# Performance work log

Measured on AMD Instinct MI355X. Metric: run time of the kernel, lower is better.

The kernel has to match this reference:

```python
import jax, jax.numpy as jnp
import numpy as np

N_NODES = 100000
N_EDGES = 3200000
HID = 128
NUM_ATTR = 10000
K = 3
EPS = 1e-5


def setup_inputs() -> dict:
    key = jax.random.key(0)
    ks = jax.random.split(key, 8)
    x_idx = jax.random.randint(ks[0], (N_NODES,), 0, NUM_ATTR)
    edge_index = jax.random.randint(ks[1], (2, N_EDGES), 0, N_NODES)
    edge_weight = jax.random.uniform(ks[2], (N_EDGES,), dtype=jnp.float32)
    emb = jax.random.normal(ks[3], (NUM_ATTR, HID), dtype=jnp.float32) * 0.1
    Wt = jax.random.normal(ks[4], (K, HID, HID), dtype=jnp.float32) * (1.0 / np.sqrt(HID))
    bt = jnp.zeros((K, HID), jnp.float32)
    Wc = jax.random.normal(ks[5], (K, 2 * HID, HID), dtype=jnp.float32) * (1.0 / np.sqrt(2 * HID))
    bc = jnp.zeros((K, HID), jnp.float32)
    cg_gamma = jnp.ones((K, HID), jnp.float32)
    cg_beta = jnp.zeros((K, HID), jnp.float32)
    cg_alpha = jnp.ones((K, HID), jnp.float32)
    gn_gamma = jnp.ones((K - 1, HID), jnp.float32)
    gn_beta = jnp.zeros((K - 1, HID), jnp.float32)
    gn_alpha = jnp.ones((K - 1, HID), jnp.float32)
    return dict(x_idx=x_idx, edge_index=edge_index, edge_weight=edge_weight, emb=emb,
                Wt=Wt, bt=bt, Wc=Wc, bc=bc, cg_gamma=cg_gamma, cg_beta=cg_beta,
                cg_alpha=cg_alpha, gn_gamma=gn_gamma, gn_beta=gn_beta, gn_alpha=gn_alpha)


def graph_norm(x, gamma, beta, alpha):
    # GraphNorm over node dim: out = gamma*(x - alpha*mean)/sqrt(var+eps) + beta
    mean = jnp.mean(x, axis=0, keepdims=True)
    sub = x - alpha * mean
    var = jnp.mean(sub * sub, axis=0, keepdims=True)
    return gamma * sub * jax.lax.rsqrt(var + EPS) + beta


def build_mean_adj_weights(edge_index, edge_weight, n_nodes):
    # aggr='mean': w_e = edge_weight_e / deg[row_e], deg from row sums (deg<0.5 -> +1)
    row = edge_index[0]
    deg = jax.ops.segment_sum(edge_weight, row, num_segments=n_nodes)
    deg = jnp.where(deg < 0.5, deg + 1.0, deg)
    inv_deg = 1.0 / deg
    return edge_weight * inv_deg[row]


def conv_layer(x_, row, col, w, Wt, bt, Wc, bc, g, b, a):
    h = jax.nn.relu(x_ @ Wt + bt)                                   # [N, HID]
    m = jax.ops.segment_sum(w[:, None] * h[col], row, num_segments=x_.shape[0])  # adj @ h
    m = graph_norm(m, g, b, a)
    return jnp.concatenate([m, x_], axis=-1) @ Wc + bc


def reference(x_idx, edge_index, edge_weight, emb, Wt, bt, Wc, bc,
              cg_gamma, cg_beta, cg_alpha, gn_gamma, gn_beta, gn_alpha):
    row, col = edge_index[0], edge_index[1]
    w = build_mean_adj_weights(edge_index, edge_weight, x_idx.shape[0])
    x = emb[x_idx]  # embedding lookup; dropout p=0 -> identity
    for i in range(K - 1):
        x = conv_layer(x, row, col, w, Wt[i], bt[i], Wc[i], bc[i],
                       cg_gamma[i], cg_beta[i], cg_alpha[i])
        x = graph_norm(x, gn_gamma[i], gn_beta[i], gn_alpha[i])
        x = jax.nn.relu(x)
    x = conv_layer(x, row, col, w, Wt[K - 1], bt[K - 1], Wc[K - 1], bc[K - 1],
                   cg_gamma[K - 1], cg_beta[K - 1], cg_alpha[K - 1])
    return x
```

## Files before the change

### kernel.cpp

```cpp
#include <hip/hip_runtime.h>
#include <cstdio>


#define HID 128

typedef __attribute__((ext_vector_type(8))) short short8;
typedef __attribute__((ext_vector_type(4))) float floatx4;
typedef __attribute__((ext_vector_type(8))) _Float16 half8;
typedef __attribute__((ext_vector_type(2))) _Float16 half2v;

__device__ __forceinline__ unsigned short f2bf(float f) {
    unsigned u = __float_as_uint(f);
    unsigned r = (u + 0x7FFFu + ((u >> 16) & 1u)) >> 16;
    return (unsigned short)r;
}
__device__ __forceinline__ float bflo(unsigned u) { return __uint_as_float(u << 16); }
__device__ __forceinline__ float bfhi(unsigned u) { return __uint_as_float(u & 0xFFFF0000u); }

#define NB 512
#define RPB 196
#define CAPB 8192
#define TILE_A 2048

__global__ __launch_bounds__(256) void k_binA(
    const int* __restrict__ row, const int* __restrict__ col,
    const float* __restrict__ ew, int2* __restrict__ binned,
    unsigned* __restrict__ cursor, int E) {
    __shared__ int2 stag[TILE_A];
    __shared__ unsigned short bof[TILE_A];
    __shared__ unsigned hist[NB], scanned[NB], bump[NB];
    __shared__ int delta[NB];
    __shared__ unsigned scanw[256];
    int t = threadIdx.x;
    int tileBase = blockIdx.x * TILE_A;
    int tcnt = min(TILE_A, E - tileBase);

    hist[t] = 0; hist[t + 256] = 0;
    __syncthreads();

    int myb[8]; int2 myv[8];
#pragma unroll
    for (int i = 0; i < 8; ++i) {
        int idx = t + i * 256;
        if (idx < tcnt) {
            int e = tileBase + idx;
            int r = row[e];
            int c = col[e];
            float w = ew[e];
            int b = r / RPB;
            int rl = r - b * RPB;
            myb[i] = b;
            myv[i] = make_int2((rl << 17) | c, __float_as_int(w));
            atomicAdd(&hist[b], 1u);
        } else {
            myb[i] = -1;
            myv[i] = make_int2(0, 0);
        }
    }
    __syncthreads();

    unsigned h0 = hist[2 * t], h1 = hist[2 * t + 1];
    unsigned p = h0 + h1;
    scanw[t] = p;
    __syncthreads();
    for (int o = 1; o < 256; o <<= 1) {
        unsigned x = (t >= o) ? scanw[t - o] : 0u;
        __syncthreads();
        scanw[t] += x;
        __syncthreads();
    }
    unsigned excl = scanw[t] - p;
    scanned[2 * t] = excl;          bump[2 * t] = excl;
    scanned[2 * t + 1] = excl + h0; bump[2 * t + 1] = excl + h0;
    __syncthreads();

#pragma unroll
    for (int j = 0; j < 2; ++j) {
        int b = t + j * 256;
        unsigned c = hist[b];
        if (c) {
            unsigned old = atomicAdd(&cursor[b], c);
            delta[b] = (int)((unsigned)b * CAPB + old) - (int)scanned[b];
        }
    }
    __syncthreads();

#pragma unroll
    for (int i = 0; i < 8; ++i) {
        if (myb[i] >= 0) {
            unsigned s = atomicAdd(&bump[myb[i]], 1u);
            stag[s] = myv[i];
            bof[s] = (unsigned short)myb[i];
        }
    }
    __syncthreads();

    for (int i = t; i < tcnt; i += 256) {
        int b = bof[i];
        int dst = delta[b] + i;
        if (dst < (b + 1) * CAPB) binned[dst] = stag[i];
    }
}

__global__ void k_bscan(const unsigned* __restrict__ cursor, unsigned* __restrict__ outbase) {
    __shared__ unsigned scanw[256];
    int t = threadIdx.x;
    unsigned h0 = min(cursor[2 * t], (unsigned)CAPB);
    unsigned h1 = min(cursor[2 * t + 1], (unsigned)CAPB);
    unsigned p = h0 + h1;
    scanw[t] = p;
    __syncthreads();
    for (int o = 1; o < 256; o <<= 1) {
        unsigned x = (t >= o) ? scanw[t - o] : 0u;
        __syncthreads();
        scanw[t] += x;
        __syncthreads();
    }
    unsigned excl = scanw[t] - p;
    outbase[2 * t] = excl;
    outbase[2 * t + 1] = excl + h0;
}

__global__ __launch_bounds__(256) void k_binB(
    const int2* __restrict__ binned, const unsigned* __restrict__ cursor,
    const unsigned* __restrict__ outbase, int2* __restrict__ edge_s,
    unsigned* __restrict__ endp, unsigned* __restrict__ cntg, int N) {
    __shared__ unsigned hist[256], bump[256], scanw[256];
    __shared__ float wsum[256], inv[256];
    int b = blockIdx.x, t = threadIdx.x;
    size_t base_in = (size_t)b * CAPB;
    unsigned cntb = min(cursor[b], (unsigned)CAPB);
    unsigned outb = outbase[b];

    hist[t] = 0;
    wsum[t] = 0.f;
    __syncthreads();
    for (unsigned i = t; i < cntb; i += 256) {
        int2 v = binned[base_in + i];
        unsigned rl = ((unsigned)v.x) >> 17;
        atomicAdd(&hist[rl], 1u);
        atomicAdd(&wsum[rl], __int_as_float(v.y));
    }
    __syncthreads();

    unsigned h = hist[t];
    scanw[t] = h;
    __syncthreads();
    for (int o = 1; o < 256; o <<= 1) {
        unsigned x = (t >= o) ? scanw[t - o] : 0u;
        __syncthreads();
        scanw[t] += x;
        __syncthreads();
    }
    unsigned excl = scanw[t] - h;
    bump[t] = excl;
    float d = wsum[t];
    d = (d < 0.5f) ? d + 1.0f : d;
    inv[t] = 1.0f / d;
    int grow = b * RPB + t;
    if (t < RPB && grow < N) {
        endp[grow] = outb + excl + h;
        cntg[grow] = h;
    }
    __syncthreads();

    for (unsigned i = t; i < cntb; i += 256) {
        int2 v = binned[base_in + i];
        unsigned rl = ((unsigned)v.x) >> 17;
        unsigned pos = outb + atomicAdd(&bump[rl], 1u);
        float w = __int_as_float(v.y) * inv[rl];
        edge_s[pos] = make_int2(v.x & 0x1FFFF, __float_as_int(w));
    }
}

__global__ void k_prepw(const float* __restrict__ Wt, const float* __restrict__ Wc,
                        unsigned short* __restrict__ WtT, unsigned short* __restrict__ WcT) {
    int tid = blockIdx.x * blockDim.x + threadIdx.x;
    const int T1 = 3 * 128 * 128;
    const int T2 = 3 * 256 * 128;
    if (tid < T1) {
        int l = tid >> 14, rem = tid & 16383;
        int n = rem >> 7, k = rem & 127;
        WtT[tid] = f2bf(Wt[l * 16384 + k * 128 + n]);
    } else if (tid < T1 + T2) {
        int t2 = tid - T1;
        int l = t2 >> 15, rem = t2 & 32767;
        int n = rem >> 8, k = rem & 255;
        WcT[t2] = f2bf(Wc[l * 32768 + k * 128 + n]);
    }
}

#define GM_ROWS 128
#define LDSP 136

__global__ __launch_bounds__(256) void k_gemm(
    const float* __restrict__ X1, const int* __restrict__ G1,
    const float* __restrict__ AB1, int relu1, int x1_f16,
    const float* __restrict__ X2, const int* __restrict__ G2,
    const float* __restrict__ AB2, int relu2,
    const unsigned short* __restrict__ Wn, int Kpitch, int nstage,
    const float* __restrict__ bias, void* __restrict__ Y, int relu_out, int out_bf16,
    float* __restrict__ Sout, int N) {
    __shared__ unsigned short Ws[128 * LDSP];
    __shared__ unsigned short Xs[128 * LDSP];
    __shared__ float sred[4][256];
    int t = threadIdx.x;
    int rowBase = blockIdx.x * GM_ROWS;
    int lane = t & 63, wave = t >> 6;
    int quad = lane >> 4, l16 = lane & 15;

    floatx4 acc[2][8];
#pragma unroll
    for (int i = 0; i < 2; ++i)
#pragma unroll
        for (int j = 0; j < 8; ++j) acc[i][j] = (floatx4){0.f, 0.f, 0.f, 0.f};

    int kg = (t & 15) * 8;
    int r0 = t >> 4;

    for (int s = 0; s < nstage; ++s) {
        const float* Xp = s ? X2 : X1;
        const int* Gp = s ? G2 : G1;
        const float* ABp = s ? AB2 : AB1;
        int rl = s ? relu2 : relu1;
        int koff = s * 128;

#pragma unroll
        for (int j = 0; j < 8; ++j) {
            int n = r0 + 16 * j;
            *(short8*)&Ws[n * LDSP + kg] =
                *(const short8*)&Wn[(size_t)n * Kpitch + koff + kg];
        }
        floatx4 Av0 = {1.f, 1.f, 1.f, 1.f}, Av1 = Av0;
        floatx4 Bv0 = {0.f, 0.f, 0.f, 0.f}, Bv1 = Bv0;
        if (ABp) {
            Av0 = *(const floatx4*)&ABp[kg];
            Av1 = *(const floatx4*)&ABp[kg + 4];
            Bv0 = *(const floatx4*)&ABp[HID + kg];
            Bv1 = *(const floatx4*)&ABp[HID + kg + 4];
        }
#pragma unroll
        for (int j = 0; j < 8; ++j) {
            int r = r0 + 16 * j;
            int grow = rowBase + r;
            floatx4 x0 = {0.f, 0.f, 0.f, 0.f}, x1 = x0;
            if (grow < N) {
                size_t srow = Gp ? (size_t)Gp[grow] : (size_t)grow;
                if (x1_f16 && s == 0) {
                    half8 mv = *(const half8*)&((const _Float16*)X1)[srow * HID + kg];
#pragma unroll
                    for (int c = 0; c < 4; ++c) {
                        x0[c] = (float)mv[c];
                        x1[c] = (float)mv[c + 4];
                    }
                } else {
                    x0 = *(const floatx4*)&Xp[srow * HID + kg];
                    x1 = *(const floatx4*)&Xp[srow * HID + kg + 4];
                }
            }
            if (ABp) {
#pragma unroll
                for (int c = 0; c < 4; ++c) {
                    x0[c] = fmaf(x0[c], Av0[c], Bv0[c]);
                    x1[c] = fmaf(x1[c], Av1[c], Bv1[c]);
                }
                if (rl) {
#pragma unroll
                    for (int c = 0; c < 4; ++c) {
                        x0[c] = fmaxf(x0[c], 0.f);
                        x1[c] = fmaxf(x1[c], 0.f);
                    }
                }
            }
            short8 st;
            st[0] = (short)f2bf(x0[0]); st[1] = (short)f2bf(x0[1]);
            st[2] = (short)f2bf(x0[2]); st[3] = (short)f2bf(x0[3]);
            st[4] = (short)f2bf(x1[0]); st[5] = (short)f2bf(x1[1]);
            st[6] = (short)f2bf(x1[2]); st[7] = (short)f2bf(x1[3]);
            *(short8*)&Xs[r * LDSP + kg] = st;
        }
        __syncthreads();

#pragma unroll
        for (int ks = 0; ks < 4; ++ks) {
            int kb = ks * 32 + quad * 8;
            short8 a0 = *(const short8*)&Xs[(wave * 32 + l16) * LDSP + kb];
            short8 a1 = *(const short8*)&Xs[(wave * 32 + 16 + l16) * LDSP + kb];
#pragma unroll
            for (int ni = 0; ni < 8; ++ni) {
                short8 b = *(const short8*)&Ws[(ni * 16 + l16) * LDSP + kb];
                acc[0][ni] = __builtin_amdgcn_mfma_f32_16x16x32_bf16(a0, b, acc[0][ni], 0, 0, 0);
                acc[1][ni] = __builtin_amdgcn_mfma_f32_16x16x32_bf16(a1, b, acc[1][ni], 0, 0, 0);
            }
        }
        __syncthreads();
    }

    float s1[8], s2[8];
#pragma unroll
    for (int ni = 0; ni < 8; ++ni) { s1[ni] = 0.f; s2[ni] = 0.f; }

#pragma unroll
    for (int mi = 0; mi < 2; ++mi) {
#pragma unroll
        for (int ni = 0; ni < 8; ++ni) {
            int gcol = ni * 16 + l16;
            float bv = bias[gcol];
#pragma unroll
            for (int reg = 0; reg < 4; ++reg) {
                int grow = rowBase + wave * 32 + mi * 16 + quad * 4 + reg;
                if (grow < N) {
                    float v = acc[mi][ni][reg] + bv;
                    if (relu_out) v = fmaxf(v, 0.f);
                    s1[ni] += v;
                    s2[ni] += v * v;
                    if (out_bf16)
                        ((unsigned short*)Y)[(size_t)grow * HID + gcol] = f2bf(v);
                    else
                        ((float*)Y)[(size_t)grow * HID + gcol] = v;
                }
            }
        }
    }

    if (Sout) {
#pragma unroll
        for (int ni = 0; ni < 8; ++ni) {
            s1[ni] += __shfl_xor(s1[ni], 16);
            s1[ni] += __shfl_xor(s1[ni], 32);
            s2[ni] += __shfl_xor(s2[ni], 16);
            s2[ni] += __shfl_xor(s2[ni], 32);
        }
        if (lane < 16) {
#pragma unroll
            for (int ni = 0; ni < 8; ++ni) {
                sred[wave][ni * 16 + l16] = s1[ni];
                sred[wave][128 + ni * 16 + l16] = s2[ni];
            }
        }
        __syncthreads();
        float v = sred[0][t & 255];
        if (t < 256) {
            v = sred[0][t] + sred[1][t] + sred[2][t] + sred[3][t];
            atomicAdd(&Sout[(blockIdx.x & 15) * 256 + t], v);
        }
    }
}

#define AGG_R 4

__global__ __launch_bounds__(256) void k_agg(
    const unsigned short* __restrict__ H, const int2* __restrict__ es,
    const unsigned* __restrict__ endp, const unsigned* __restrict__ cnt,
    _Float16* __restrict__ Mh, float* __restrict__ Spart, int N) {
    __shared__ float sb[4][256];
    int t = threadIdx.x;
    int wv = t >> 6, lane = t & 63;
    int grp = lane >> 4;
    int l16 = lane & 15;
    const uint4* __restrict__ H4 = (const uint4*)H;
    int rowBase = blockIdx.x * (4 * AGG_R) + wv * AGG_R;
    int fo = l16 * 8 + grp * 2;
    float s1a = 0.f, s1b = 0.f, s2a = 0.f, s2b = 0.f;

    for (int j = 0; j < AGG_R; ++j) {
        int rowi = rowBase + j;
        if (rowi >= N) break;
        unsigned e = endp[rowi];
        unsigned p = e - cnt[rowi];

        float acc[8];
#pragma unroll
        for (int i = 0; i < 8; ++i) acc[i] = 0.f;

        for (; p + 15 < e; p += 16) {
            int2 ee[4];
#pragma unroll
            for (int q = 0; q < 4; ++q) ee[q] = es[p + 4 * q + grp];
            uint4 hh[4];
#pragma unroll
            for (int q = 0; q < 4; ++q)
                hh[q] = H4[(size_t)ee[q].x * 16 + l16];
            __builtin_amdgcn_sched_barrier(0);
#pragma unroll
            for (int q = 0; q < 4; ++q) {
                float w = __int_as_float(ee[q].y);
                acc[0] = fmaf(w, bflo(hh[q].x), acc[0]);
                acc[1] = fmaf(w, bfhi(hh[q].x), acc[1]);
                acc[2] = fmaf(w, bflo(hh[q].y), acc[2]);
                acc[3] = fmaf(w, bfhi(hh[q].y), acc[3]);
                acc[4] = fmaf(w, bflo(hh[q].z), acc[4]);
                acc[5] = fmaf(w, bfhi(hh[q].z), acc[5]);
                acc[6] = fmaf(w, bflo(hh[q].w), acc[6]);
                acc[7] = fmaf(w, bfhi(hh[q].w), acc[7]);
            }
        }
        for (; p < e; p += 4) {
            unsigned idx = p + grp;
            int2 e0 = make_int2(0, 0);
            if (idx < e) e0 = es[idx];
            uint4 h = H4[(size_t)e0.x * 16 + l16];
            float w = __int_as_float(e0.y);
            acc[0] = fmaf(w, bflo(h.x), acc[0]);
            acc[1] = fmaf(w, bfhi(h.x), acc[1]);
            acc[2] = fmaf(w, bflo(h.y), acc[2]);
            acc[3] = fmaf(w, bfhi(h.y), acc[3]);
            acc[4] = fmaf(w, bflo(h.z), acc[4]);
            acc[5] = fmaf(w, bfhi(h.z), acc[5]);
            acc[6] = fmaf(w, bflo(h.w), acc[6]);
            acc[7] = fmaf(w, bfhi(h.w), acc[7]);
        }

#pragma unroll
        for (int i = 0; i < 8; ++i) {
            acc[i] += __shfl_xor(acc[i], 16);
            acc[i] += __shfl_xor(acc[i], 32);
        }
        float va = (grp & 2) ? ((grp & 1) ? acc[6] : acc[4])
                             : ((grp & 1) ? acc[2] : acc[0]);
        float vb = (grp & 2) ? ((grp & 1) ? acc[7] : acc[5])
                             : ((grp & 1) ? acc[3] : acc[1]);
        half2v st;
        st[0] = (_Float16)va;
        st[1] = (_Float16)vb;
        *(half2v*)&Mh[(size_t)rowi * HID + fo] = st;
        s1a += va; s1b += vb;
        s2a += va * va; s2b += vb * vb;
    }

    sb[wv][fo] = s1a;
    sb[wv][fo + 1] = s1b;
    sb[wv][128 + fo] = s2a;
    sb[wv][128 + fo + 1] = s2b;
    __syncthreads();
    {
        float v = sb[0][t] + sb[1][t] + sb[2][t] + sb[3][t];
        atomicAdd(&Spart[(blockIdx.x & 15) * 256 + t], v);
    }
}

__global__ void k_finalize(const float* __restrict__ S, const float* __restrict__ gamma,
                           const float* __restrict__ beta, const float* __restrict__ alpha,
                           float* __restrict__ AB, float invN) {
    int f = threadIdx.x;
    float sum = 0.f, sq = 0.f;
#pragma unroll
    for (int c = 0; c < 16; ++c) {
        sum += S[c * 256 + f];
        sq += S[c * 256 + 128 + f];
    }
    float mu = sum * invN;
    float ex2 = sq * invN;
    float a = alpha[f];
    float var = ex2 - 2.f * a * mu * mu + a * a * mu * mu;
    float rs = rsqrtf(var + 1e-5f);
    float A = gamma[f] * rs;
    float B = beta[f] - A * a * mu;
    AB[f] = A;
    AB[HID + f] = B;
}

extern "C" void kernel_launch(void* const* d_in, const int* in_sizes, int n_in,
                              void* d_out, int out_size, void* d_ws, size_t ws_size,
                              hipStream_t stream) {
    const int*   x_idx = (const int*)d_in[0];
    const int*   ei    = (const int*)d_in[1];
    const float* ew    = (const float*)d_in[2];
    const float* emb   = (const float*)d_in[3];
    const float* Wt    = (const float*)d_in[4];
    const float* bt    = (const float*)d_in[5];
    const float* Wc    = (const float*)d_in[6];
    const float* bc    = (const float*)d_in[7];
    const float* cg_g  = (const float*)d_in[8];
    const float* cg_b  = (const float*)d_in[9];
    const float* cg_a  = (const float*)d_in[10];
    const float* gn_g  = (const float*)d_in[11];
    const float* gn_b  = (const float*)d_in[12];
    const float* gn_a  = (const float*)d_in[13];
    const int N = in_sizes[0];
    const int E = in_sizes[2];
    const int* row = ei;
    const int* col = ei + E;

    char* ws = (char*)d_ws;
    size_t off = 0;
    auto alloc = [&](size_t bytes) -> void* {
        size_t o = (off + 511) & ~(size_t)511;
        off = o + bytes;
        return (void*)(ws + o);
    };
    const int SSTRIDE = 16 * 256;
    unsigned* cursor = (unsigned*)alloc(NB * 4);
    float*    Spart  = (float*)alloc(5 * SSTRIDE * 4);
    size_t zero_end = off;
    unsigned* outbase = (unsigned*)alloc(NB * 4);
    unsigned* endp    = (unsigned*)alloc((size_t)N * 4);
    unsigned* cnt     = (unsigned*)alloc((size_t)N * 4);
    float*    AB      = (float*)alloc(5 * 256 * 4);
    unsigned short* WtT = (unsigned short*)alloc((size_t)3 * 128 * 128 * 2);
    unsigned short* WcT = (unsigned short*)alloc((size_t)3 * 128 * 256 * 2);
    int2*     binned  = (int2*)alloc((size_t)NB * CAPB * 8);
    int2*     edge_s  = (int2*)alloc((size_t)E * 8);
    unsigned short* H = (unsigned short*)alloc((size_t)N * HID * 2);
    float*    X       = (float*)alloc((size_t)N * HID * 4);
    _Float16* Mh      = (_Float16*)alloc((size_t)N * HID * 2);
    if (off > ws_size) {
        fprintf(stderr, "kernel_launch: ws too small (%zu > %zu)\n", off, ws_size);
        return;
    }

    hipMemsetAsync(d_ws, 0, zero_end, stream);

    k_prepw<<<(3 * 128 * 128 + 3 * 256 * 128 + 255) / 256, 256, 0, stream>>>(Wt, Wc, WtT, WcT);
    k_binA<<<(E + TILE_A - 1) / TILE_A, 256, 0, stream>>>(row, col, ew, binned, cursor, E);
    k_bscan<<<1, 256, 0, stream>>>(cursor, outbase);
    k_binB<<<NB, 256, 0, stream>>>(binned, cursor, outbase, edge_s, endp, cnt, N);

    int gemm_blocks = (N + GM_ROWS - 1) / GM_ROWS;
    auto gemm = [&](const float* X1, const int* G1, const float* AB1, int rl1, int xf16,
                    const float* X2, const int* G2, const float* AB2, int rl2,
                    const unsigned short* Wn, int Kpitch, int nstage,
                    const float* bias, void* Y, int relu_out, int out_bf16,
                    float* Sout) {
        k_gemm<<<gemm_blocks, 256, 0, stream>>>(X1, G1, AB1, rl1, xf16, X2, G2, AB2, rl2,
                                                Wn, Kpitch, nstage, bias, Y,
                                                relu_out, out_bf16, Sout, N);
    };
    int aggB = (N + 4 * AGG_R - 1) / (4 * AGG_R);
    auto agg = [&](int stage) {
        k_agg<<<aggB, 256, 0, stream>>>(H, edge_s, endp, cnt, Mh,
                                        Spart + stage * SSTRIDE, N);
    };
    auto fin = [&](int stage, const float* g, const float* b, const float* a) {
        k_finalize<<<1, 128, 0, stream>>>(Spart + stage * SSTRIDE, g, b, a,
                                          AB + stage * 256, 1.0f / (float)N);
    };

    gemm(emb, x_idx, nullptr, 0, 0, nullptr, nullptr, nullptr, 0, WtT, 128, 1, bt,
         H, 1, 1, nullptr);
    agg(0);
    fin(0, cg_g, cg_b, cg_a);
    gemm((const float*)Mh, nullptr, AB + 0 * 256, 0, 1, emb, x_idx, nullptr, 0,
         WcT, 256, 2, bc, X, 0, 0, Spart + 1 * SSTRIDE);
    fin(1, gn_g, gn_b, gn_a);

    gemm(X, nullptr, AB + 1 * 256, 1, 0, nullptr, nullptr, nullptr, 0,
         WtT + 16384, 128, 1, bt + 128, H, 1, 1, nullptr);
    agg(2);
    fin(2, cg_g + 128, cg_b + 128, cg_a + 128);
    gemm((const float*)Mh, nullptr, AB + 2 * 256, 0, 1, X, nullptr, AB + 1 * 256, 1,
         WcT + 32768, 256, 2, bc + 128, X, 0, 0, Spart + 3 * SSTRIDE);
    fin(3, gn_g + 128, gn_b + 128, gn_a + 128);

    gemm(X, nullptr, AB + 3 * 256, 1, 0, nullptr, nullptr, nullptr, 0,
         WtT + 2 * 16384, 128, 1, bt + 256, H, 1, 1, nullptr);
    agg(4);
    fin(4, cg_g + 256, cg_b + 256, cg_a + 256);
    gemm((const float*)Mh, nullptr, AB + 4 * 256, 0, 1, X, nullptr, AB + 3 * 256, 1,
         WcT + 2 * 32768, 256, 2, bc + 256, d_out, 0, 0, nullptr);
}
```

Baseline: 769.4 us.

## Fuse norm finalize and bin scan into consumers; store intermediate X in fp16

Drops the separate bin-scan kernel: every k_binB block now recomputes the 512-entry prefix scan in shared memory. Drops the five k_finalize launches: each GEMM computes the GraphNorm scale and shift from the partial sums in its prologue. The inter-layer activation X is stored as fp16 instead of fp32, which halves its write and read traffic. The cost is redundant per-block scan and finalize work, plus lower precision for the intermediate activations.

```diff
diff --git a/kernel.cpp b/kernel.cpp
--- a/kernel.cpp
+++ b/kernel.cpp
@@ -102,35 +102,35 @@
     }
 }
 
-__global__ void k_bscan(const unsigned* __restrict__ cursor, unsigned* __restrict__ outbase) {
-    __shared__ unsigned scanw[256];
-    int t = threadIdx.x;
-    unsigned h0 = min(cursor[2 * t], (unsigned)CAPB);
-    unsigned h1 = min(cursor[2 * t + 1], (unsigned)CAPB);
-    unsigned p = h0 + h1;
-    scanw[t] = p;
-    __syncthreads();
-    for (int o = 1; o < 256; o <<= 1) {
-        unsigned x = (t >= o) ? scanw[t - o] : 0u;
-        __syncthreads();
-        scanw[t] += x;
-        __syncthreads();
-    }
-    unsigned excl = scanw[t] - p;
-    outbase[2 * t] = excl;
-    outbase[2 * t + 1] = excl + h0;
-}
-
 __global__ __launch_bounds__(256) void k_binB(
     const int2* __restrict__ binned, const unsigned* __restrict__ cursor,
-    const unsigned* __restrict__ outbase, int2* __restrict__ edge_s,
-    unsigned* __restrict__ endp, unsigned* __restrict__ cntg, int N) {
+    int2* __restrict__ edge_s, unsigned* __restrict__ endp,
+    unsigned* __restrict__ cntg, int N) {
     __shared__ unsigned hist[256], bump[256], scanw[256];
     __shared__ float wsum[256], inv[256];
+    __shared__ unsigned sc[NB];
     int b = blockIdx.x, t = threadIdx.x;
+
+    {
+        unsigned h0 = min(cursor[2 * t], (unsigned)CAPB);
+        unsigned h1 = min(cursor[2 * t + 1], (unsigned)CAPB);
+        unsigned p = h0 + h1;
+        scanw[t] = p;
+        __syncthreads();
+        for (int o = 1; o < 256; o <<= 1) {
+            unsigned x = (t >= o) ? scanw[t - o] : 0u;
+            __syncthreads();
+            scanw[t] += x;
+            __syncthreads();
+        }
+        unsigned excl = scanw[t] - p;
+        sc[2 * t] = excl;
+        sc[2 * t + 1] = excl + h0;
+        __syncthreads();
+    }
+    unsigned outb = sc[b];
     size_t base_in = (size_t)b * CAPB;
     unsigned cntb = min(cursor[b], (unsigned)CAPB);
-    unsigned outb = outbase[b];
 
     hist[t] = 0;
     wsum[t] = 0.f;
@@ -195,20 +195,55 @@
 
 __global__ __launch_bounds__(256) void k_gemm(
     const float* __restrict__ X1, const int* __restrict__ G1,
-    const float* __restrict__ AB1, int relu1, int x1_f16,
+    const float* __restrict__ S1, const float* __restrict__ g1,
+    const float* __restrict__ b1, const float* __restrict__ a1,
+    int relu1, int xf1,
     const float* __restrict__ X2, const int* __restrict__ G2,
-    const float* __restrict__ AB2, int relu2,
+    const float* __restrict__ S2, const float* __restrict__ g2,
+    const float* __restrict__ b2, const float* __restrict__ a2,
+    int relu2, int xf2,
     const unsigned short* __restrict__ Wn, int Kpitch, int nstage,
-    const float* __restrict__ bias, void* __restrict__ Y, int relu_out, int out_bf16,
-    float* __restrict__ Sout, int N) {
+    const float* __restrict__ bias, void* __restrict__ Y,
+    int relu_out, int out_mode, float* __restrict__ Sout,
+    float invN, int N) {
     __shared__ unsigned short Ws[128 * LDSP];
     __shared__ unsigned short Xs[128 * LDSP];
     __shared__ float sred[4][256];
+    __shared__ float ABs[2][256];
     int t = threadIdx.x;
     int rowBase = blockIdx.x * GM_ROWS;
     int lane = t & 63, wave = t >> 6;
     int quad = lane >> 4, l16 = lane & 15;
 
+    if (S1 && t < 128) {
+        float sum = 0.f, sq = 0.f;
+#pragma unroll
+        for (int c = 0; c < 16; ++c) {
+            sum += S1[c * 256 + t];
+            sq += S1[c * 256 + 128 + t];
+        }
+        float mu = sum * invN, ex2 = sq * invN, al = a1[t];
+        float var = ex2 - 2.f * al * mu * mu + al * al * mu * mu;
+        float A = g1[t] * rsqrtf(var + 1e-5f);
+        ABs[0][t] = A;
+        ABs[0][128 + t] = b1[t] - A * al * mu;
+    }
+    if (S2 && t >= 128) {
+        int f = t - 128;
+        float sum = 0.f, sq = 0.f;
+#pragma unroll
+        for (int c = 0; c < 16; ++c) {
+            sum += S2[c * 256 + f];
+            sq += S2[c * 256 + 128 + f];
+        }
+        float mu = sum * invN, ex2 = sq * invN, al = a2[f];
+        float var = ex2 - 2.f * al * mu * mu + al * al * mu * mu;
+        float A = g2[f] * rsqrtf(var + 1e-5f);
+        ABs[1][f] = A;
+        ABs[1][128 + f] = b2[f] - A * al * mu;
+    }
+    __syncthreads();
+
     floatx4 acc[2][8];
 #pragma unroll
     for (int i = 0; i < 2; ++i)
@@ -221,8 +256,10 @@
     for (int s = 0; s < nstage; ++s) {
         const float* Xp = s ? X2 : X1;
         const int* Gp = s ? G2 : G1;
-        const float* ABp = s ? AB2 : AB1;
+        const float* ABp = s ? (S2 ? (const float*)ABs[1] : (const float*)nullptr)
+                             : (S1 ? (const float*)ABs[0] : (const float*)nullptr);
         int rl = s ? relu2 : relu1;
+        int xf = s ? xf2 : xf1;
         int koff = s * 128;
 
 #pragma unroll
@@ -246,8 +283,8 @@
             floatx4 x0 = {0.f, 0.f, 0.f, 0.f}, x1 = x0;
             if (grow < N) {
                 size_t srow = Gp ? (size_t)Gp[grow] : (size_t)grow;
-                if (x1_f16 && s == 0) {
-                    half8 mv = *(const half8*)&((const _Float16*)X1)[srow * HID + kg];
+                if (xf) {
+                    half8 mv = *(const half8*)&((const _Float16*)Xp)[srow * HID + kg];
 #pragma unroll
                     for (int c = 0; c < 4; ++c) {
                         x0[c] = (float)mv[c];
@@ -314,8 +351,10 @@
                     if (relu_out) v = fmaxf(v, 0.f);
                     s1[ni] += v;
                     s2[ni] += v * v;
-                    if (out_bf16)
+                    if (out_mode == 1)
                         ((unsigned short*)Y)[(size_t)grow * HID + gcol] = f2bf(v);
+                    else if (out_mode == 2)
+                        ((_Float16*)Y)[(size_t)grow * HID + gcol] = (_Float16)v;
                     else
                         ((float*)Y)[(size_t)grow * HID + gcol] = v;
                 }
@@ -437,27 +476,6 @@
         float v = sb[0][t] + sb[1][t] + sb[2][t] + sb[3][t];
         atomicAdd(&Spart[(blockIdx.x & 15) * 256 + t], v);
     }
-}
-
-__global__ void k_finalize(const float* __restrict__ S, const float* __restrict__ gamma,
-                           const float* __restrict__ beta, const float* __restrict__ alpha,
-                           float* __restrict__ AB, float invN) {
-    int f = threadIdx.x;
-    float sum = 0.f, sq = 0.f;
-#pragma unroll
-    for (int c = 0; c < 16; ++c) {
-        sum += S[c * 256 + f];
-        sq += S[c * 256 + 128 + f];
-    }
-    float mu = sum * invN;
-    float ex2 = sq * invN;
-    float a = alpha[f];
-    float var = ex2 - 2.f * a * mu * mu + a * a * mu * mu;
-    float rs = rsqrtf(var + 1e-5f);
-    float A = gamma[f] * rs;
-    float B = beta[f] - A * a * mu;
-    AB[f] = A;
-    AB[HID + f] = B;
 }
 
 extern "C" void kernel_launch(void* const* d_in, const int* in_sizes, int n_in,
@@ -493,16 +511,14 @@
     unsigned* cursor = (unsigned*)alloc(NB * 4);
     float*    Spart  = (float*)alloc(5 * SSTRIDE * 4);
     size_t zero_end = off;
-    unsigned* outbase = (unsigned*)alloc(NB * 4);
     unsigned* endp    = (unsigned*)alloc((size_t)N * 4);
     unsigned* cnt     = (unsigned*)alloc((size_t)N * 4);
-    float*    AB      = (float*)alloc(5 * 256 * 4);
     unsigned short* WtT = (unsigned short*)alloc((size_t)3 * 128 * 128 * 2);
     unsigned short* WcT = (unsigned short*)alloc((size_t)3 * 128 * 256 * 2);
     int2*     binned  = (int2*)alloc((size_t)NB * CAPB * 8);
     int2*     edge_s  = (int2*)alloc((size_t)E * 8);
     unsigned short* H = (unsigned short*)alloc((size_t)N * HID * 2);
-    float*    X       = (float*)alloc((size_t)N * HID * 4);
+    _Float16* Xh      = (_Float16*)alloc((size_t)N * HID * 2);
     _Float16* Mh      = (_Float16*)alloc((size_t)N * HID * 2);
     if (off > ws_size) {
         fprintf(stderr, "kernel_launch: ws too small (%zu > %zu)\n", off, ws_size);
@@ -513,49 +529,49 @@
 
     k_prepw<<<(3 * 128 * 128 + 3 * 256 * 128 + 255) / 256, 256, 0, stream>>>(Wt, Wc, WtT, WcT);
     k_binA<<<(E + TILE_A - 1) / TILE_A, 256, 0, stream>>>(row, col, ew, binned, cursor, E);
-    k_bscan<<<1, 256, 0, stream>>>(cursor, outbase);
-    k_binB<<<NB, 256, 0, stream>>>(binned, cursor, outbase, edge_s, endp, cnt, N);
+    k_binB<<<NB, 256, 0, stream>>>(binned, cursor, edge_s, endp, cnt, N);
 
     int gemm_blocks = (N + GM_ROWS - 1) / GM_ROWS;
-    auto gemm = [&](const float* X1, const int* G1, const float* AB1, int rl1, int xf16,
-                    const float* X2, const int* G2, const float* AB2, int rl2,
+    float invN = 1.0f / (float)N;
+    auto gemm = [&](const float* X1, const int* G1, const float* S1,
+                    const float* g1, const float* b1, const float* a1, int rl1, int xf1,
+                    const float* X2, const int* G2, const float* S2,
+                    const float* g2, const float* b2, const float* a2, int rl2, int xf2,
                     const unsigned short* Wn, int Kpitch, int nstage,
-                    const float* bias, void* Y, int relu_out, int out_bf16,
+                    const float* bias, void* Y, int relu_out, int out_mode,
                     float* Sout) {
-        k_gemm<<<gemm_blocks, 256, 0, stream>>>(X1, G1, AB1, rl1, xf16, X2, G2, AB2, rl2,
-                                                Wn, Kpitch, nstage, bias, Y,
-                                                relu_out, out_bf16, Sout, N);
+        k_gemm<<<gemm_blocks, 256, 0, stream>>>(
+            X1, G1, S1, g1, b1, a1, rl1, xf1,
+            X2, G2, S2, g2, b2, a2, rl2, xf2,
+            Wn, Kpitch, nstage, bias, Y, relu_out, out_mode, Sout, invN, N);
     };
     int aggB = (N + 4 * AGG_R - 1) / (4 * AGG_R);
     auto agg = [&](int stage) {
         k_agg<<<aggB, 256, 0, stream>>>(H, edge_s, endp, cnt, Mh,
                                         Spart + stage * SSTRIDE, N);
     };
-    auto fin = [&](int stage, const float* g, const float* b, const float* a) {
-        k_finalize<<<1, 128, 0, stream>>>(Spart + stage * SSTRIDE, g, b, a,
-                                          AB + stage * 256, 1.0f / (float)N);
-    };
-
-    gemm(emb, x_idx, nullptr, 0, 0, nullptr, nullptr, nullptr, 0, WtT, 128, 1, bt,
-         H, 1, 1, nullptr);
+
+    gemm(emb, x_idx, nullptr, nullptr, nullptr, nullptr, 0, 0,
+         nullptr, nullptr, nullptr, nullptr, nullptr, nullptr, 0, 0,
+         WtT, 128, 1, bt, H, 1, 1, nullptr);
     agg(0);
-    fin(0, cg_g, cg_b, cg_a);
-    gemm((const float*)Mh, nullptr, AB + 0 * 256, 0, 1, emb, x_idx, nullptr, 0,
-         WcT, 256, 2, bc, X, 0, 0, Spart + 1 * SSTRIDE);
-    fin(1, gn_g, gn_b, gn_a);
-
-    gemm(X, nullptr, AB + 1 * 256, 1, 0, nullptr, nullptr, nullptr, 0,
+    gemm((const float*)Mh, nullptr, Spart + 0 * SSTRIDE, cg_g, cg_b, cg_a, 0, 1,
+         emb, x_idx, nullptr, nullptr, nullptr, nullptr, 0, 0,
+         WcT, 256, 2, bc, Xh, 0, 2, Spart + 1 * SSTRIDE);
+
+    gemm((const float*)Xh, nullptr, Spart + 1 * SSTRIDE, gn_g, gn_b, gn_a, 1, 1,
+         nullptr, nullptr, nullptr, nullptr, nullptr, nullptr, 0, 0,
          WtT + 16384, 128, 1, bt + 128, H, 1, 1, nullptr);
     agg(2);
-    fin(2, cg_g + 128, cg_b + 128, cg_a + 128);
-    gemm((const float*)Mh, nullptr, AB + 2 * 256, 0, 1, X, nullptr, AB + 1 * 256, 1,
-         WcT + 32768, 256, 2, bc + 128, X, 0, 0, Spart + 3 * SSTRIDE);
-    fin(3, gn_g + 128, gn_b + 128, gn_a + 128);
-
-    gemm(X, nullptr, AB + 3 * 256, 1, 0, nullptr, nullptr, nullptr, 0,
+    gemm((const float*)Mh, nullptr, Spart + 2 * SSTRIDE, cg_g + 128, cg_b + 128, cg_a + 128, 0, 1,
+         (const float*)Xh, nullptr, Spart + 1 * SSTRIDE, gn_g, gn_b, gn_a, 1, 1,
+         WcT + 32768, 256, 2, bc + 128, Xh, 0, 2, Spart + 3 * SSTRIDE);
+
+    gemm((const float*)Xh, nullptr, Spart + 3 * SSTRIDE, gn_g + 128, gn_b + 128, gn_a + 128, 1, 1,
+         nullptr, nullptr, nullptr, nullptr, nullptr, nullptr, 0, 0,
          WtT + 2 * 16384, 128, 1, bt + 256, H, 1, 1, nullptr);
     agg(4);
-    fin(4, cg_g + 256, cg_b + 256, cg_a + 256);
-    gemm((const float*)Mh, nullptr, AB + 4 * 256, 0, 1, X, nullptr, AB + 3 * 256, 1,
+    gemm((const float*)Mh, nullptr, Spart + 4 * SSTRIDE, cg_g + 256, cg_b + 256, cg_a + 256, 0, 1,
+         (const float*)Xh, nullptr, Spart + 3 * SSTRIDE, gn_g + 128, gn_b + 128, gn_a + 128, 1, 1,
          WcT + 2 * 32768, 256, 2, bc + 256, d_out, 0, 0, nullptr);
 }
```

Result: no change. 784.7 us (+2.0%).
